# Optimization experiments

Hardware: AMD Instinct MI355X
Metric: run time of the kernel (lower is better)

Reference implementation:

```python
import jax, jax.numpy as jnp
import numpy as np

SWIGLU_ALPHA = 1.702
SWIGLU_LIMIT = 7.0
B, S, H, E, K, I = 2, 2048, 2048, 32, 4, 1024


def setup_inputs() -> dict:
    key = jax.random.key(0)
    ks = jax.random.split(key, 8)
    return {
        "hidden_states": jax.random.normal(ks[0], (B, S, H), jnp.float32),
        "gate_w": jax.random.normal(ks[1], (E, H), jnp.float32) * 0.02,
        "gate_b": jnp.zeros((E,), jnp.float32),
        "w_gate": jax.random.normal(ks[2], (E, H, I), jnp.float32) * 0.02,
        "b_gate": jnp.zeros((E, I), jnp.float32),
        "w_up": jax.random.normal(ks[3], (E, H, I), jnp.float32) * 0.02,
        "b_up": jnp.zeros((E, I), jnp.float32),
        "w_down": jax.random.normal(ks[4], (E, I, H), jnp.float32) * 0.02,
        "b_down": jnp.zeros((E, H), jnp.float32),
    }


def reference(hidden_states, gate_w, gate_b, w_gate, b_gate, w_up, b_up, w_down, b_down):
    Bb, Ss, Hh = hidden_states.shape
    x = hidden_states.reshape(-1, Hh)                      # [T, H]
    # --- gate: top-k logits first, then softmax over the selected subset ---
    logits = x @ gate_w.T + gate_b                         # [T, E]
    topk_logits, topk_idx = jax.lax.top_k(logits, K)       # sorted descending
    topk_weight = jax.nn.softmax(topk_logits.astype(jnp.float32), axis=-1)  # [T, K]
    # --- dispatch: replicate each token K times, sort by expert id ---
    flat_idx = topk_idx.reshape(-1)                        # [T*K]
    xs = jnp.repeat(x, K, axis=0)                          # [T*K, H]
    order = jnp.argsort(flat_idx)                          # stable sort by expert
    xt = xs[order]
    gid = flat_idx[order]                                  # expert id per sorted row
    group_sizes = jnp.bincount(flat_idx, length=E).astype(jnp.int32)
    # --- grouped GEMM experts with GPT-OSS SwiGLU ---
    gate = jax.lax.ragged_dot(xt, w_gate, group_sizes) + b_gate[gid]
    up = jax.lax.ragged_dot(xt, w_up, group_sizes) + b_up[gid]
    gate = jnp.minimum(gate, SWIGLU_LIMIT)
    up = jnp.clip(up, -SWIGLU_LIMIT, SWIGLU_LIMIT)
    glu = gate * jax.nn.sigmoid(SWIGLU_ALPHA * gate)
    activated = (up + 1.0) * glu
    outs = jax.lax.ragged_dot(activated, w_down, group_sizes) + b_down[gid]
    # --- unsort and combine with routing weights ---
    inv = jnp.argsort(order)
    outs = outs[inv].reshape(-1, K, Hh)                    # [T, K, H]
    y = jnp.sum(outs * topk_weight[..., None], axis=1).astype(x.dtype)
    return y.reshape(Bb, Ss, Hh)
```

## Files before the change

### kernel.cpp

```cpp
#include <hip/hip_runtime.h>

#define T_TOK 4096
#define E_EXP 32
#define HDIM  2048
#define IDIM  1024
#define TKROW 16384
#define BM    256
#define MAXT  96

typedef __attribute__((ext_vector_type(8))) short   short8;
typedef __attribute__((ext_vector_type(8))) __bf16  bf16x8;
typedef __attribute__((ext_vector_type(4))) float   f32x4;

typedef const __attribute__((address_space(1))) unsigned int* gas_t;
typedef __attribute__((address_space(3))) unsigned int*       las_t;

static __device__ __forceinline__ void gload16(const void* g, void* l) {
    __builtin_amdgcn_global_load_lds((gas_t)(uintptr_t)g, (las_t)(uintptr_t)l, 16, 0, 0);
}

static __device__ __forceinline__ f32x4 mfma16(short8 a, short8 b, f32x4 c) {
    return __builtin_amdgcn_mfma_f32_16x16x32_bf16(
        __builtin_bit_cast(bf16x8, a), __builtin_bit_cast(bf16x8, b), c, 0, 0, 0);
}

static __device__ __forceinline__ unsigned short f2bf(float f) {
    unsigned u = __builtin_bit_cast(unsigned, f);
    unsigned r = (u + 0x7FFFu + ((u >> 16) & 1u)) >> 16;
    return (unsigned short)r;
}
static __device__ __forceinline__ float bf2f(unsigned short u) {
    return __builtin_bit_cast(float, ((unsigned)u) << 16);
}
static __device__ __forceinline__ unsigned cvtpk(float lo, float hi) {
    unsigned r;
    asm("v_cvt_pk_bf16_f32 %0, %1, %2" : "=v"(r) : "v"(lo), "v"(hi));
    return r;
}

#define VM0()   asm volatile("s_waitcnt vmcnt(0)" ::: "memory")
#define LGKM0() asm volatile("s_waitcnt lgkmcnt(0)" ::: "memory")

__global__ __launch_bounds__(256) void gating_kernel(
    const float* __restrict__ x, const float* __restrict__ gw,
    const float* __restrict__ gb, int* __restrict__ topk_idx,
    float* __restrict__ topk_w)
{
    int wave = threadIdx.x >> 6, lane = threadIdx.x & 63;
    int t = blockIdx.x * 4 + wave;
    const float* xr = x + (size_t)t * HDIM;
    float xv[32];
#pragma unroll
    for (int j = 0; j < 32; j++) xv[j] = xr[lane + 64 * j];
    float logits[E_EXP];
#pragma unroll
    for (int e = 0; e < E_EXP; e++) {
        const float* wr = gw + (size_t)e * HDIM;
        float s = 0.f;
#pragma unroll
        for (int j = 0; j < 32; j++) s = fmaf(xv[j], wr[lane + 64 * j], s);
#pragma unroll
        for (int off = 32; off; off >>= 1) s += __shfl_xor(s, off);
        logits[e] = s + gb[e];
    }
    unsigned sel = 0;
    float v[4]; int id[4];
#pragma unroll
    for (int kk = 0; kk < 4; kk++) {
        float best = -3.4e38f; int bi = 0;
#pragma unroll
        for (int e = 0; e < E_EXP; e++) {
            bool ok = ((sel >> e) & 1u) == 0u;
            bool gt = ok && (logits[e] > best);
            best = gt ? logits[e] : best;
            bi   = gt ? e : bi;
        }
        sel |= 1u << bi; v[kk] = best; id[kk] = bi;
    }
    float m0 = v[0];
    float e0 = __expf(v[0] - m0), e1 = __expf(v[1] - m0);
    float e2 = __expf(v[2] - m0), e3 = __expf(v[3] - m0);
    float inv = 1.f / (e0 + e1 + e2 + e3);
    if (lane == 0) {
        int b4 = t * 4;
        topk_idx[b4 + 0] = id[0]; topk_w[b4 + 0] = e0 * inv;
        topk_idx[b4 + 1] = id[1]; topk_w[b4 + 1] = e1 * inv;
        topk_idx[b4 + 2] = id[2]; topk_w[b4 + 2] = e2 * inv;
        topk_idx[b4 + 3] = id[3]; topk_w[b4 + 3] = e3 * inv;
    }
}

__global__ void init_kernel(int* counts, int* fill) {
    if (threadIdx.x < E_EXP) { counts[threadIdx.x] = 0; fill[threadIdx.x] = 0; }
}

__global__ void histo_kernel(const int* __restrict__ idx, int* counts) {
    int i = blockIdx.x * 256 + threadIdx.x;
    atomicAdd(&counts[idx[i]], 1);
}

__global__ void scan_tiles_kernel(const int* counts, int* offsets,
                                  int* tile_e, int* tile_r, int* ntiles) {
    if (threadIdx.x == 0) {
        int acc = 0;
        for (int e = 0; e < E_EXP; e++) { offsets[e] = acc; acc += counts[e]; }
        offsets[E_EXP] = acc;
        int nt = 0;
        for (int e = 0; e < E_EXP; e++) {
            int c = counts[e];
            for (int r = 0; r < c; r += BM) {
                tile_e[nt] = e; tile_r[nt] = offsets[e] + r; nt++;
            }
        }
        ntiles[0] = nt;
    }
}

__global__ void scatter_kernel(const int* __restrict__ idx, const int* __restrict__ offsets,
                               int* fill, int* __restrict__ pos_of, int* __restrict__ row_tok) {
    int i = blockIdx.x * 256 + threadIdx.x;
    int e = idx[i];
    int pos = offsets[e] + atomicAdd(&fill[e], 1);
    pos_of[i] = pos;
    row_tok[pos] = i >> 2;
}

__global__ __launch_bounds__(64) void gather_kernel(
    const float* __restrict__ x, const int* __restrict__ row_tok,
    unsigned short* __restrict__ xt)
{
    int r = blockIdx.x, lane = threadIdx.x;
    const f32x4* src = (const f32x4*)(x + (size_t)row_tok[r] * HDIM);
    unsigned short* dst = xt + (size_t)r * HDIM;
#pragma unroll
    for (int j = 0; j < 8; j++) {
        f32x4 f = src[lane + 64 * j];
        uint2 o;
        o.x = cvtpk(f[0], f[1]);
        o.y = cvtpk(f[2], f[3]);
        *(uint2*)(dst + 4 * (lane + 64 * j)) = o;
    }
}

__global__ __launch_bounds__(512, 2) void gemm1_kernel(
    const unsigned short* __restrict__ xt, const float* __restrict__ w_gate,
    const float* __restrict__ b_gate, const float* __restrict__ w_up,
    const float* __restrict__ b_up, const int* __restrict__ tile_e,
    const int* __restrict__ tile_r, const int* __restrict__ ntiles,
    const int* __restrict__ offsets, const int* __restrict__ counts,
    unsigned short* __restrict__ act)
{
    int flat = blockIdx.y * 8 + blockIdx.x;
    int swz = (flat & 7) * (MAXT * 8 / 8) + (flat >> 3);
    int tid = swz >> 3, nb = swz & 7;
    if (tid >= ntiles[0]) return;
    int e = tile_e[tid], row0 = tile_r[tid];
    int cnt_end = offsets[e] + counts[e];
    int n0 = nb * 128;

    __shared__ unsigned short As[2][BM * 64];
    __shared__ unsigned short Bgs[2][128 * 64];
    __shared__ unsigned short Bus[2][128 * 64];

    int t = threadIdx.x, lane = t & 63, w = t >> 6;
    int wr = w >> 2, wc = w & 3;
    int lrow = lane & 15, lg8 = (lane >> 4) * 8;

    f32x4 accg[8][2], accu[8][2];
#pragma unroll
    for (int m = 0; m < 8; m++)
#pragma unroll
        for (int n = 0; n < 2; n++) { accg[m][n] = (f32x4)0.f; accu[m][n] = (f32x4)0.f; }

    int arow_l = (lane >> 3);
    int achunk = (lane & 7) ^ arow_l;
    int bn = (t & 31) * 4, bk = (t >> 5) * 4;
    int bfswz = ((t & 31) & 7) << 3;
    size_t wB = (size_t)e * ((size_t)HDIM * IDIM) + (size_t)bk * IDIM + n0 + bn;

    f32x4 gReg[4], uReg[4];

#define G1_STAGE_A(KT, BUF) do { int k0_ = (KT) * 64; \
    _Pragma("unroll") for (int i_ = 0; i_ < 4; i_++) { \
        int ar_ = row0 + 32 * w + 8 * i_ + arow_l; \
        if (ar_ > TKROW - 1) ar_ = TKROW - 1; \
        gload16(xt + (size_t)ar_ * HDIM + k0_ + achunk * 8, \
                (void*)&As[BUF][(32 * w + 8 * i_) * 64]); \
    } } while (0)

#define G1_LOADB(KT) do { \
    const float* gp_ = w_gate + wB + (size_t)(KT) * 64 * IDIM; \
    const float* up_ = w_up   + wB + (size_t)(KT) * 64 * IDIM; \
    _Pragma("unroll") for (int kk_ = 0; kk_ < 4; kk_++) { \
        gReg[kk_] = *(const f32x4*)(gp_ + (size_t)kk_ * IDIM); \
        uReg[kk_] = *(const f32x4*)(up_ + (size_t)kk_ * IDIM); \
    } } while (0)

#define G1_WRITEB(BUF) do { \
    _Pragma("unroll") for (int j_ = 0; j_ < 4; j_++) { \
        uint2 vg_, vu_; \
        vg_.x = cvtpk(gReg[0][j_], gReg[1][j_]); vg_.y = cvtpk(gReg[2][j_], gReg[3][j_]); \
        vu_.x = cvtpk(uReg[0][j_], uReg[1][j_]); vu_.y = cvtpk(uReg[2][j_], uReg[3][j_]); \
        int d_ = (bn + j_) * 64 + (bk ^ bfswz); \
        *(uint2*)&Bgs[BUF][d_] = vg_; *(uint2*)&Bus[BUF][d_] = vu_; \
    } } while (0)

#define G1_MFMA(BUF) do { \
    __builtin_amdgcn_s_setprio(1); \
    _Pragma("unroll") for (int kk_ = 0; kk_ < 2; kk_++) { \
        short8 af_[8], bg_[2], bu_[2]; \
        int ke_ = kk_ * 32 + lg8; \
        _Pragma("unroll") for (int m_ = 0; m_ < 8; m_++) \
            af_[m_] = *(const short8*)&As[BUF][(wr * 128 + m_ * 16 + lrow) * 64 + (ke_ ^ ((lrow & 7) << 3))]; \
        _Pragma("unroll") for (int n_ = 0; n_ < 2; n_++) { \
            int rb_ = wc * 32 + n_ * 16 + lrow; \
            int d_ = rb_ * 64 + (ke_ ^ (((rb_ >> 2) & 7) << 3)); \
            bg_[n_] = *(const short8*)&Bgs[BUF][d_]; \
            bu_[n_] = *(const short8*)&Bus[BUF][d_]; \
        } \
        _Pragma("unroll") for (int m_ = 0; m_ < 8; m_++) \
        _Pragma("unroll") for (int n_ = 0; n_ < 2; n_++) { \
            accg[m_][n_] = mfma16(af_[m_], bg_[n_], accg[m_][n_]); \
            accu[m_][n_] = mfma16(af_[m_], bu_[n_], accu[m_][n_]); \
        } \
    } \
    __builtin_amdgcn_s_setprio(0); } while (0)

    G1_STAGE_A(0, 0);
    G1_LOADB(0);
    VM0();
    G1_WRITEB(0);
    LGKM0();
    __builtin_amdgcn_s_barrier();

    int cur = 0;
#pragma unroll 1
    for (int kt = 0; kt < 32; kt++) {
        if (kt + 1 < 32) { G1_STAGE_A(kt + 1, cur ^ 1); G1_LOADB(kt + 1); }
        G1_MFMA(cur);
        VM0();
        if (kt + 1 < 32) G1_WRITEB(cur ^ 1);
        LGKM0();
        __builtin_amdgcn_s_barrier();
        cur ^= 1;
    }
#undef G1_STAGE_A
#undef G1_LOADB
#undef G1_WRITEB
#undef G1_MFMA

#pragma unroll
    for (int nf = 0; nf < 2; nf++) {
        int col = n0 + wc * 32 + nf * 16 + lrow;
        float bgv = b_gate[e * IDIM + col];
        float buv = b_up[e * IDIM + col];
#pragma unroll
        for (int m = 0; m < 8; m++) {
            int rb = row0 + wr * 128 + m * 16 + (lane >> 4) * 4;
#pragma unroll
            for (int r = 0; r < 4; r++) {
                int grow = rb + r;
                if (grow < cnt_end) {
                    float gv = accg[m][nf][r] + bgv;
                    float uv = accu[m][nf][r] + buv;
                    gv = fminf(gv, 7.f);
                    uv = fminf(fmaxf(uv, -7.f), 7.f);
                    float glu = gv / (1.f + __expf(-1.702f * gv));
                    act[(size_t)grow * IDIM + col] = f2bf((uv + 1.f) * glu);
                }
            }
        }
    }
}

__global__ __launch_bounds__(512, 2) void gemm2_kernel(
    const unsigned short* __restrict__ actb, const float* __restrict__ w_down,
    const float* __restrict__ b_down, const int* __restrict__ tile_e,
    const int* __restrict__ tile_r, const int* __restrict__ ntiles,
    const int* __restrict__ offsets, const int* __restrict__ counts,
    unsigned short* __restrict__ outs)
{
    int flat = blockIdx.y * 8 + blockIdx.x;
    int swz = (flat & 7) * (MAXT * 8 / 8) + (flat >> 3);
    int tid = swz >> 3, nb = swz & 7;
    if (tid >= ntiles[0]) return;
    int e = tile_e[tid], row0 = tile_r[tid];
    int cnt_end = offsets[e] + counts[e];
    int n0 = nb * 256;

    __shared__ unsigned short As[2][BM * 64];
    __shared__ unsigned short Bs[2][256 * 64];

    int t = threadIdx.x, lane = t & 63, w = t >> 6;
    int wr = w >> 2, wc = w & 3;
    int lrow = lane & 15, lg8 = (lane >> 4) * 8;

    f32x4 acc[8][4];
#pragma unroll
    for (int m = 0; m < 8; m++)
#pragma unroll
        for (int n = 0; n < 4; n++) acc[m][n] = (f32x4)0.f;

    int arow_l = (lane >> 3);
    int achunk = (lane & 7) ^ arow_l;
    int bn = (t & 63) * 4, bk = w * 8;
    int bfswz = (lane & 7) << 3;
    size_t wB = (size_t)e * ((size_t)IDIM * HDIM) + (size_t)bk * HDIM + n0 + bn;

    f32x4 dReg[8];

#define G2_STAGE_A(KT, BUF) do { int k0_ = (KT) * 64; \
    _Pragma("unroll") for (int i_ = 0; i_ < 4; i_++) { \
        int ar_ = row0 + 32 * w + 8 * i_ + arow_l; \
        if (ar_ > TKROW - 1) ar_ = TKROW - 1; \
        gload16(actb + (size_t)ar_ * IDIM + k0_ + achunk * 8, \
                (void*)&As[BUF][(32 * w + 8 * i_) * 64]); \
    } } while (0)

#define G2_LOADB(KT) do { \
    const float* gp_ = w_down + wB + (size_t)(KT) * 64 * HDIM; \
    _Pragma("unroll") for (int kk_ = 0; kk_ < 8; kk_++) \
        dReg[kk_] = *(const f32x4*)(gp_ + (size_t)kk_ * HDIM); \
    } while (0)

#define G2_WRITEB(BUF) do { \
    _Pragma("unroll") for (int j_ = 0; j_ < 4; j_++) { \
        uint4 v_; \
        v_.x = cvtpk(dReg[0][j_], dReg[1][j_]); v_.y = cvtpk(dReg[2][j_], dReg[3][j_]); \
        v_.z = cvtpk(dReg[4][j_], dReg[5][j_]); v_.w = cvtpk(dReg[6][j_], dReg[7][j_]); \
        int d_ = (bn + j_) * 64 + (bk ^ bfswz); \
        *(uint4*)&Bs[BUF][d_] = v_; \
    } } while (0)

#define G2_MFMA(BUF) do { \
    __builtin_amdgcn_s_setprio(1); \
    _Pragma("unroll") for (int kk_ = 0; kk_ < 2; kk_++) { \
        short8 af_[8], bf_[4]; \
        int ke_ = kk_ * 32 + lg8; \
        _Pragma("unroll") for (int m_ = 0; m_ < 8; m_++) \
            af_[m_] = *(const short8*)&As[BUF][(wr * 128 + m_ * 16 + lrow) * 64 + (ke_ ^ ((lrow & 7) << 3))]; \
        _Pragma("unroll") for (int n_ = 0; n_ < 4; n_++) { \
            int rb_ = wc * 64 + n_ * 16 + lrow; \
            bf_[n_] = *(const short8*)&Bs[BUF][rb_ * 64 + (ke_ ^ (((rb_ >> 2) & 7) << 3))]; \
        } \
        _Pragma("unroll") for (int m_ = 0; m_ < 8; m_++) \
        _Pragma("unroll") for (int n_ = 0; n_ < 4; n_++) \
            acc[m_][n_] = mfma16(af_[m_], bf_[n_], acc[m_][n_]); \
    } \
    __builtin_amdgcn_s_setprio(0); } while (0)

    G2_STAGE_A(0, 0);
    G2_LOADB(0);
    VM0();
    G2_WRITEB(0);
    LGKM0();
    __builtin_amdgcn_s_barrier();

    int cur = 0;
#pragma unroll 1
    for (int kt = 0; kt < 16; kt++) {
        if (kt + 1 < 16) { G2_STAGE_A(kt + 1, cur ^ 1); G2_LOADB(kt + 1); }
        G2_MFMA(cur);
        VM0();
        if (kt + 1 < 16) G2_WRITEB(cur ^ 1);
        LGKM0();
        __builtin_amdgcn_s_barrier();
        cur ^= 1;
    }
#undef G2_STAGE_A
#undef G2_LOADB
#undef G2_WRITEB
#undef G2_MFMA

#pragma unroll
    for (int nf = 0; nf < 4; nf++) {
        int col = n0 + wc * 64 + nf * 16 + lrow;
        float bdv = b_down[e * HDIM + col];
#pragma unroll
        for (int m = 0; m < 8; m++) {
            int rb = row0 + wr * 128 + m * 16 + (lane >> 4) * 4;
#pragma unroll
            for (int r = 0; r < 4; r++) {
                int grow = rb + r;
                if (grow < cnt_end)
                    outs[(size_t)grow * HDIM + col] = f2bf(acc[m][nf][r] + bdv);
            }
        }
    }
}

__global__ __launch_bounds__(256) void combine_kernel(
    const unsigned short* __restrict__ outs, const int* __restrict__ pos_of,
    const float* __restrict__ topk_w, float* __restrict__ y)
{
    int tok = blockIdx.x;
    int c0 = threadIdx.x * 8;
    float acc[8] = {0.f, 0.f, 0.f, 0.f, 0.f, 0.f, 0.f, 0.f};
#pragma unroll
    for (int k = 0; k < 4; k++) {
        int pos = pos_of[tok * 4 + k];
        float w = topk_w[tok * 4 + k];
        short8 vv = *(const short8*)(outs + (size_t)pos * HDIM + c0);
#pragma unroll
        for (int j = 0; j < 8; j++)
            acc[j] = fmaf(w, bf2f((unsigned short)vv[j]), acc[j]);
    }
    float4 o0 = make_float4(acc[0], acc[1], acc[2], acc[3]);
    float4 o1 = make_float4(acc[4], acc[5], acc[6], acc[7]);
    *(float4*)(y + (size_t)tok * HDIM + c0)     = o0;
    *(float4*)(y + (size_t)tok * HDIM + c0 + 4) = o1;
}

extern "C" void kernel_launch(void* const* d_in, const int* in_sizes, int n_in,
                              void* d_out, int out_size, void* d_ws, size_t ws_size,
                              hipStream_t stream) {
    const float* x      = (const float*)d_in[0];
    const float* gw     = (const float*)d_in[1];
    const float* gb     = (const float*)d_in[2];
    const float* w_gate = (const float*)d_in[3];
    const float* b_gate = (const float*)d_in[4];
    const float* w_up   = (const float*)d_in[5];
    const float* b_up   = (const float*)d_in[6];
    const float* w_down = (const float*)d_in[7];
    const float* b_down = (const float*)d_in[8];
    float* y = (float*)d_out;

    char* base = (char*)d_ws;
    size_t off = 0;
    int*   topk_idx = (int*)(base + off);   off += (size_t)TKROW * 4;
    float* topk_w   = (float*)(base + off); off += (size_t)TKROW * 4;
    int*   counts   = (int*)(base + off);   off += 256;
    int*   offsets  = (int*)(base + off);   off += 256;
    int*   fill     = (int*)(base + off);   off += 256;
    int*   ntiles   = (int*)(base + off);   off += 256;
    int*   tile_e   = (int*)(base + off);   off += 1024;
    int*   tile_r   = (int*)(base + off);   off += 1024;
    int*   pos_of   = (int*)(base + off);   off += (size_t)TKROW * 4;
    int*   row_tok  = (int*)(base + off);   off += (size_t)TKROW * 4;
    unsigned short* xt   = (unsigned short*)(base + off); off += (size_t)TKROW * HDIM * 2;
    unsigned short* act  = (unsigned short*)(base + off); off += (size_t)TKROW * IDIM * 2;
    unsigned short* outs = (unsigned short*)(base + off); off += (size_t)TKROW * HDIM * 2;

    init_kernel<<<1, 64, 0, stream>>>(counts, fill);
    gating_kernel<<<T_TOK / 4, 256, 0, stream>>>(x, gw, gb, topk_idx, topk_w);
    histo_kernel<<<TKROW / 256, 256, 0, stream>>>(topk_idx, counts);
    scan_tiles_kernel<<<1, 64, 0, stream>>>(counts, offsets, tile_e, tile_r, ntiles);
    scatter_kernel<<<TKROW / 256, 256, 0, stream>>>(topk_idx, offsets, fill, pos_of, row_tok);
    gather_kernel<<<TKROW, 64, 0, stream>>>(x, row_tok, xt);
    gemm1_kernel<<<dim3(8, MAXT), 512, 0, stream>>>(
        xt, w_gate, b_gate, w_up, b_up, tile_e, tile_r, ntiles, offsets, counts, act);
    gemm2_kernel<<<dim3(8, MAXT), 512, 0, stream>>>(
        act, w_down, b_down, tile_e, tile_r, ntiles, offsets, counts, outs);
    combine_kernel<<<T_TOK, 256, 0, stream>>>(outs, pos_of, topk_w, y);
}
```

Before: 622.6 us.

## Restructure gating with LDS token tiles and fuse histogram and scatter-gather

The gating kernel now processes 8 tokens per 1024-thread block. Each token tile is staged in LDS, and each wave keeps two expert weight rows in registers, so the gate weights are read from global memory far fewer times. The expert histogram is folded into gating via atomics, and the scatter and gather kernels are merged so each wave computes its destination row and copies the token directly. This removes two launches and the row_tok intermediate. In exchange, row order within each expert now depends on atomic timing, and the swizzle expression is only simplified.

Measured after the change: 645.7 us. 1.04x slower.

```diff
diff --git a/kernel.cpp b/kernel.cpp
--- a/kernel.cpp
+++ b/kernel.cpp
@@ -41,62 +41,84 @@
 #define VM0()   asm volatile("s_waitcnt vmcnt(0)" ::: "memory")
 #define LGKM0() asm volatile("s_waitcnt lgkmcnt(0)" ::: "memory")
 
-__global__ __launch_bounds__(256) void gating_kernel(
+__global__ __launch_bounds__(1024) void gating_kernel(
     const float* __restrict__ x, const float* __restrict__ gw,
     const float* __restrict__ gb, int* __restrict__ topk_idx,
-    float* __restrict__ topk_w)
+    float* __restrict__ topk_w, int* __restrict__ counts)
 {
-    int wave = threadIdx.x >> 6, lane = threadIdx.x & 63;
-    int t = blockIdx.x * 4 + wave;
-    const float* xr = x + (size_t)t * HDIM;
-    float xv[32];
-#pragma unroll
-    for (int j = 0; j < 32; j++) xv[j] = xr[lane + 64 * j];
-    float logits[E_EXP];
-#pragma unroll
-    for (int e = 0; e < E_EXP; e++) {
-        const float* wr = gw + (size_t)e * HDIM;
-        float s = 0.f;
-#pragma unroll
-        for (int j = 0; j < 32; j++) s = fmaf(xv[j], wr[lane + 64 * j], s);
-#pragma unroll
-        for (int off = 32; off; off >>= 1) s += __shfl_xor(s, off);
-        logits[e] = s + gb[e];
-    }
-    unsigned sel = 0;
-    float v[4]; int id[4];
-#pragma unroll
-    for (int kk = 0; kk < 4; kk++) {
-        float best = -3.4e38f; int bi = 0;
-#pragma unroll
-        for (int e = 0; e < E_EXP; e++) {
-            bool ok = ((sel >> e) & 1u) == 0u;
-            bool gt = ok && (logits[e] > best);
-            best = gt ? logits[e] : best;
-            bi   = gt ? e : bi;
+    __shared__ float xs[8][HDIM];
+    __shared__ float L[8][34];
+    int t = threadIdx.x, lane = t & 63, w = t >> 6;
+    int tok0 = blockIdx.x * 8;
+
+    const f32x4* src = (const f32x4*)(x + (size_t)tok0 * HDIM);
+    f32x4* dst = (f32x4*)&xs[0][0];
+#pragma unroll
+    for (int j = 0; j < 4; j++) dst[t + 1024 * j] = src[t + 1024 * j];
+
+    f32x4 wr0[8], wr1[8];
+    {
+        const f32x4* g0 = (const f32x4*)(gw + (size_t)(2 * w) * HDIM);
+        const f32x4* g1 = (const f32x4*)(gw + (size_t)(2 * w + 1) * HDIM);
+#pragma unroll
+        for (int j = 0; j < 8; j++) { wr0[j] = g0[lane + 64 * j]; wr1[j] = g1[lane + 64 * j]; }
+    }
+    float b0 = gb[2 * w], b1 = gb[2 * w + 1];
+    __syncthreads();
+
+#pragma unroll 1
+    for (int tt = 0; tt < 8; tt++) {
+        const f32x4* xv = (const f32x4*)&xs[tt][0];
+        float d0 = 0.f, d1 = 0.f;
+#pragma unroll
+        for (int j = 0; j < 8; j++) {
+            f32x4 xx = xv[lane + 64 * j];
+            d0 = fmaf(xx[0], wr0[j][0], d0); d0 = fmaf(xx[1], wr0[j][1], d0);
+            d0 = fmaf(xx[2], wr0[j][2], d0); d0 = fmaf(xx[3], wr0[j][3], d0);
+            d1 = fmaf(xx[0], wr1[j][0], d1); d1 = fmaf(xx[1], wr1[j][1], d1);
+            d1 = fmaf(xx[2], wr1[j][2], d1); d1 = fmaf(xx[3], wr1[j][3], d1);
         }
-        sel |= 1u << bi; v[kk] = best; id[kk] = bi;
-    }
-    float m0 = v[0];
-    float e0 = __expf(v[0] - m0), e1 = __expf(v[1] - m0);
-    float e2 = __expf(v[2] - m0), e3 = __expf(v[3] - m0);
-    float inv = 1.f / (e0 + e1 + e2 + e3);
-    if (lane == 0) {
-        int b4 = t * 4;
+#pragma unroll
+        for (int off = 32; off; off >>= 1) { d0 += __shfl_xor(d0, off); d1 += __shfl_xor(d1, off); }
+        if (lane == 0) { L[tt][2 * w] = d0 + b0; L[tt][2 * w + 1] = d1 + b1; }
+    }
+    __syncthreads();
+
+    if (w == 0 && lane < 8) {
+        int tok = tok0 + lane;
+        float lg[E_EXP];
+#pragma unroll
+        for (int e = 0; e < E_EXP; e++) lg[e] = L[lane][e];
+        unsigned sel = 0;
+        float v[4]; int id[4];
+#pragma unroll
+        for (int kk = 0; kk < 4; kk++) {
+            float best = -3.4e38f; int bi = 0;
+#pragma unroll
+            for (int e = 0; e < E_EXP; e++) {
+                bool ok = ((sel >> e) & 1u) == 0u;
+                bool gt = ok && (lg[e] > best);
+                best = gt ? lg[e] : best;
+                bi   = gt ? e : bi;
+            }
+            sel |= 1u << bi; v[kk] = best; id[kk] = bi;
+        }
+        float m0 = v[0];
+        float e0 = __expf(v[0] - m0), e1 = __expf(v[1] - m0);
+        float e2 = __expf(v[2] - m0), e3 = __expf(v[3] - m0);
+        float inv = 1.f / (e0 + e1 + e2 + e3);
+        int b4 = tok * 4;
         topk_idx[b4 + 0] = id[0]; topk_w[b4 + 0] = e0 * inv;
         topk_idx[b4 + 1] = id[1]; topk_w[b4 + 1] = e1 * inv;
         topk_idx[b4 + 2] = id[2]; topk_w[b4 + 2] = e2 * inv;
         topk_idx[b4 + 3] = id[3]; topk_w[b4 + 3] = e3 * inv;
+        atomicAdd(&counts[id[0]], 1); atomicAdd(&counts[id[1]], 1);
+        atomicAdd(&counts[id[2]], 1); atomicAdd(&counts[id[3]], 1);
     }
 }
 
 __global__ void init_kernel(int* counts, int* fill) {
     if (threadIdx.x < E_EXP) { counts[threadIdx.x] = 0; fill[threadIdx.x] = 0; }
-}
-
-__global__ void histo_kernel(const int* __restrict__ idx, int* counts) {
-    int i = blockIdx.x * 256 + threadIdx.x;
-    atomicAdd(&counts[idx[i]], 1);
 }
 
 __global__ void scan_tiles_kernel(const int* counts, int* offsets,
@@ -116,22 +138,22 @@
     }
 }
 
-__global__ void scatter_kernel(const int* __restrict__ idx, const int* __restrict__ offsets,
-                               int* fill, int* __restrict__ pos_of, int* __restrict__ row_tok) {
-    int i = blockIdx.x * 256 + threadIdx.x;
-    int e = idx[i];
-    int pos = offsets[e] + atomicAdd(&fill[e], 1);
-    pos_of[i] = pos;
-    row_tok[pos] = i >> 2;
-}
-
-__global__ __launch_bounds__(64) void gather_kernel(
-    const float* __restrict__ x, const int* __restrict__ row_tok,
-    unsigned short* __restrict__ xt)
+__global__ __launch_bounds__(256) void scatter_gather_kernel(
+    const float* __restrict__ x, const int* __restrict__ idx,
+    const int* __restrict__ offsets, int* fill,
+    int* __restrict__ pos_of, unsigned short* __restrict__ xt)
 {
-    int r = blockIdx.x, lane = threadIdx.x;
-    const f32x4* src = (const f32x4*)(x + (size_t)row_tok[r] * HDIM);
-    unsigned short* dst = xt + (size_t)r * HDIM;
+    int w = threadIdx.x >> 6, lane = threadIdx.x & 63;
+    int i = blockIdx.x * 4 + w;
+    int pos = 0;
+    if (lane == 0) {
+        int e = idx[i];
+        pos = offsets[e] + atomicAdd(&fill[e], 1);
+        pos_of[i] = pos;
+    }
+    pos = __shfl(pos, 0);
+    const f32x4* src = (const f32x4*)(x + (size_t)(i >> 2) * HDIM);
+    unsigned short* dst = xt + (size_t)pos * HDIM;
 #pragma unroll
     for (int j = 0; j < 8; j++) {
         f32x4 f = src[lane + 64 * j];
@@ -151,7 +173,7 @@
     unsigned short* __restrict__ act)
 {
     int flat = blockIdx.y * 8 + blockIdx.x;
-    int swz = (flat & 7) * (MAXT * 8 / 8) + (flat >> 3);
+    int swz = (flat & 7) * MAXT + (flat >> 3);
     int tid = swz >> 3, nb = swz & 7;
     if (tid >= ntiles[0]) return;
     int e = tile_e[tid], row0 = tile_r[tid];
@@ -281,7 +303,7 @@
     unsigned short* __restrict__ outs)
 {
     int flat = blockIdx.y * 8 + blockIdx.x;
-    int swz = (flat & 7) * (MAXT * 8 / 8) + (flat >> 3);
+    int swz = (flat & 7) * MAXT + (flat >> 3);
     int tid = swz >> 3, nb = swz & 7;
     if (tid >= ntiles[0]) return;
     int e = tile_e[tid], row0 = tile_r[tid];
@@ -436,17 +458,14 @@
     int*   tile_e   = (int*)(base + off);   off += 1024;
     int*   tile_r   = (int*)(base + off);   off += 1024;
     int*   pos_of   = (int*)(base + off);   off += (size_t)TKROW * 4;
-    int*   row_tok  = (int*)(base + off);   off += (size_t)TKROW * 4;
     unsigned short* xt   = (unsigned short*)(base + off); off += (size_t)TKROW * HDIM * 2;
     unsigned short* act  = (unsigned short*)(base + off); off += (size_t)TKROW * IDIM * 2;
     unsigned short* outs = (unsigned short*)(base + off); off += (size_t)TKROW * HDIM * 2;
 
     init_kernel<<<1, 64, 0, stream>>>(counts, fill);
-    gating_kernel<<<T_TOK / 4, 256, 0, stream>>>(x, gw, gb, topk_idx, topk_w);
-    histo_kernel<<<TKROW / 256, 256, 0, stream>>>(topk_idx, counts);
+    gating_kernel<<<T_TOK / 8, 1024, 0, stream>>>(x, gw, gb, topk_idx, topk_w, counts);
     scan_tiles_kernel<<<1, 64, 0, stream>>>(counts, offsets, tile_e, tile_r, ntiles);
-    scatter_kernel<<<TKROW / 256, 256, 0, stream>>>(topk_idx, offsets, fill, pos_of, row_tok);
-    gather_kernel<<<TKROW, 64, 0, stream>>>(x, row_tok, xt);
+    scatter_gather_kernel<<<TKROW / 4, 256, 0, stream>>>(x, topk_idx, offsets, fill, pos_of, xt);
     gemm1_kernel<<<dim3(8, MAXT), 512, 0, stream>>>(
         xt, w_gate, b_gate, w_up, b_up, tile_e, tile_r, ntiles, offsets, counts, act);
     gemm2_kernel<<<dim3(8, MAXT), 512, 0, stream>>>(
```
